# Kernel optimization log

Measured on AMD Instinct MI355X. Metric: run time of the kernel, lower is better.

Reference implementation:

```python
import jax, jax.numpy as jnp
import numpy as np

L = 6    # num_coupling_layers
D = 128  # input_dim
H = 16   # hidden width (output_dim in Coupling)
B = 131072


def setup_inputs() -> dict:
    key = jax.random.key(0)
    ks = jax.random.split(key, 32)
    half = D // 2
    m0 = np.concatenate([np.zeros(half), np.ones(half)])  # mask for even layers
    masks = jnp.asarray(np.stack([m0, 1.0 - m0] * (L // 2)), dtype=jnp.float32)  # [L, D]

    def glorot(k, shape):
        fan_in, fan_out = shape[-2], shape[-1]
        lim = np.sqrt(6.0 / (fan_in + fan_out)).astype(np.float32)
        return jax.random.uniform(k, shape, jnp.float32, -lim, lim)

    inp = {"x": jax.random.normal(ks[0], (B, D), jnp.float32), "masks": masks}
    ki = 1
    for p in ("t", "s"):
        for j, (din, dout) in enumerate([(D, H), (H, H), (H, H), (H, H), (H, D)], start=1):
            inp[f"{p}W{j}"] = glorot(ks[ki], (L, din, dout)); ki += 1
            inp[f"{p}b{j}"] = jnp.zeros((L, dout), jnp.float32)
    return inp


def _net(h, W1, b1, W2, b2, W3, b3, W4, b4, W5, b5):
    # 4 relu Dense(16) layers + linear Dense(D) head
    for W, b in ((W1, b1), (W2, b2), (W3, b3), (W4, b4)):
        h = jax.nn.relu(h @ W + b)
    return h @ W5 + b5


def _forward(x, masks, tW1, tb1, tW2, tb2, tW3, tb3, tW4, tb4, tW5, tb5,
             sW1, sb1, sW2, sb2, sW3, sb3, sW4, sb4, sW5, sb5):
    # training=True => direction = -1, gate = -1, layers iterated in reverse
    params = (masks, tW1, tb1, tW2, tb2, tW3, tb3, tW4, tb4, tW5, tb5,
              sW1, sb1, sW2, sb2, sW3, sb3, sW4, sb4, sW5, sb5)
    rev = jax.tree_util.tree_map(lambda a: a[::-1], params)  # reversed layer order

    def body(carry, p):
        x, ld = carry
        mask = p[0]
        rm = 1.0 - mask                      # reversed_mask
        xm = x * mask                        # x_masked
        t = rm * _net(xm, *p[1:11])          # translate (linear head)
        s = rm * jnp.tanh(_net(xm, *p[11:21]))  # log-scale (tanh head)
        # x = rm*(x*exp(-s) + (-1)*t*exp(-1*s)) + xm  ==  rm*(x - t)*exp(-s) + xm
        x = rm * (x - t) * jnp.exp(-s) + xm
        ld = ld - jnp.sum(s, axis=1)         # log_det_inv += gate * sum(s), gate = -1
        return (x, ld), None

    (y, logdet), _ = jax.lax.scan(body, (x, jnp.zeros(x.shape[0], x.dtype)), rev)
    return y, logdet


def reference(x, masks, tW1, tb1, tW2, tb2, tW3, tb3, tW4, tb4, tW5, tb5,
              sW1, sb1, sW2, sb2, sW3, sb3, sW4, sb4, sW5, sb5):
    return _forward(x, masks, tW1, tb1, tW2, tb2, tW3, tb3, tW4, tb4, tW5, tb5,
                    sW1, sb1, sW2, sb2, sW3, sb3, sW4, sb4, sW5, sb5)
```

## Files before the change

### kernel.cpp

```cpp
#include <hip/hip_runtime.h>
#include <math.h>

#define NL 6
#define DD 128

typedef __bf16 bf16x8 __attribute__((ext_vector_type(8)));
typedef float  f32x4  __attribute__((ext_vector_type(4)));

#define NET_STRIDE 9216
#define OFF_HID    2048
#define OFF_HEAD   5120

static __device__ __forceinline__ unsigned cvt_pk_bf16(float lo, float hi){
    unsigned r;
    asm("v_cvt_pk_bf16_f32 %0, %1, %2" : "=v"(r) : "v"(lo), "v"(hi));
    return r;
}
static __device__ __forceinline__ f32x4 mfma(bf16x8 a, bf16x8 b, f32x4 c){
    return __builtin_amdgcn_mfma_f32_16x16x32_bf16(a, b, c, 0, 0, 0);
}
static __device__ __forceinline__ bf16x8 frag4(unsigned w0, unsigned w1, unsigned w2, unsigned w3){
    int4 v; v.x=(int)w0; v.y=(int)w1; v.z=(int)w2; v.w=(int)w3;
    return __builtin_bit_cast(bf16x8, v);
}
static __device__ __forceinline__ bf16x8 dreg_to_B(f32x4 d){
    unsigned w0 = cvt_pk_bf16(fmaxf(d[0],0.f), fmaxf(d[1],0.f));
    unsigned w1 = cvt_pk_bf16(fmaxf(d[2],0.f), fmaxf(d[3],0.f));
    return frag4(w0, w1, 0u, 0u);
}
static __device__ __forceinline__ bf16x8 load_frag(const unsigned char* nb, int off, int lane){
    return *(const bf16x8*)(nb + off + lane * 16);
}

static __device__ __forceinline__ unsigned short f2bf_rne(float f){
    unsigned u = __float_as_uint(f);
    u += 0x7FFFu + ((u >> 16) & 1u);
    return (unsigned short)(u >> 16);
}

__global__ void pack_frags(
    const float* __restrict__ tW1, const float* __restrict__ tW2,
    const float* __restrict__ tW3, const float* __restrict__ tW4,
    const float* __restrict__ tW5,
    const float* __restrict__ sW1, const float* __restrict__ sW2,
    const float* __restrict__ sW3, const float* __restrict__ sW4,
    const float* __restrict__ sW5,
    unsigned char* __restrict__ pw)
{
    const int bx = blockIdx.x;
    const int l = bx >> 1, p = bx & 1;
    const int aOff = (l & 1) ? 0 : 64;
    const int pOff = 64 - aOff;
    const float* W1 = p ? sW1 : tW1;
    const float* W2 = p ? sW2 : tW2;
    const float* W3 = p ? sW3 : tW3;
    const float* W4 = p ? sW4 : tW4;
    const float* W5 = p ? sW5 : tW5;
    unsigned char* base = pw + (size_t)bx * NET_STRIDE;

    for (int t = threadIdx.x; t < 576; t += blockDim.x){
        const int lane = t & 63, m = lane & 15, q = lane >> 4;
        unsigned short v[8];
        unsigned char* dst;
        if (t < 128){
            int slice = t >> 6;
            #pragma unroll
            for (int e = 0; e < 8; ++e){
                int sg = (e < 4) ? (4*q + e) : (16 + 4*q + (e - 4));
                v[e] = f2bf_rne(W1[l*2048 + (aOff + 32*slice + sg)*16 + m]);
            }
            dst = base + slice*1024 + lane*16;
        } else if (t < 320){
            int hh = (t - 128) >> 6;
            const float* W = (hh == 0) ? W2 : (hh == 1) ? W3 : W4;
            #pragma unroll
            for (int e = 0; e < 8; ++e)
                v[e] = (e < 4) ? f2bf_rne(W[l*256 + (4*q + e)*16 + m]) : (unsigned short)0;
            dst = base + OFF_HID + hh*1024 + lane*16;
        } else {
            int c = (t - 320) >> 6;
            #pragma unroll
            for (int e = 0; e < 8; ++e)
                v[e] = (e < 4) ? f2bf_rne(W5[l*2048 + (4*q + e)*128 + pOff + 16*c + m])
                               : (unsigned short)0;
            dst = base + OFF_HEAD + c*1024 + lane*16;
        }
        int4 o;
        o.x = (int)((unsigned)v[0] | ((unsigned)v[1] << 16));
        o.y = (int)((unsigned)v[2] | ((unsigned)v[3] << 16));
        o.z = (int)((unsigned)v[4] | ((unsigned)v[5] << 16));
        o.w = (int)((unsigned)v[6] | ((unsigned)v[7] << 16));
        *(int4*)dst = o;
    }
}

__global__ __launch_bounds__(256, 6)
void realnvp_mfma16(const float* __restrict__ X, const unsigned char* __restrict__ PW,
    const float* __restrict__ tb1, const float* __restrict__ tb2,
    const float* __restrict__ tb3, const float* __restrict__ tb4,
    const float* __restrict__ tb5,
    const float* __restrict__ sb1, const float* __restrict__ sb2,
    const float* __restrict__ sb3, const float* __restrict__ sb4,
    const float* __restrict__ sb5,
    float* __restrict__ Y, float* __restrict__ LD, int B)
{
    __shared__ float4 xpl[4][256];
    const int tid  = threadIdx.x;
    const int lane = tid & 63;
    const int wid  = blockIdx.x * 4 + (tid >> 6);
    const int q = lane >> 4, n = lane & 15;
    const int row = wid * 16 + n;
    if (wid * 16 >= B) return;
    const int rowc = (row < B) ? row : (B - 1);

    const float* xrow = X + (size_t)rowc * DD;
    float4 xa[4];
    #pragma unroll
    for (int j = 0; j < 4; ++j){
        const int off = 16*j + 4*q;
        xa[j]       = *(const float4*)(xrow + off);
        xpl[j][tid] = *(const float4*)(xrow + 64 + off);
    }
    float sacc = 0.f;

    #pragma unroll 1
    for (int step = 0; step < NL; ++step){
        const int l = NL - 1 - step;
        const int pOff = (l & 1) ? 64 : 0;
        const unsigned char* bt = PW + (size_t)(l * 2 + 0) * NET_STRIDE;
        const unsigned char* bs = PW + (size_t)(l * 2 + 1) * NET_STRIDE;

        bf16x8 Bt0 = frag4(cvt_pk_bf16(xa[0].x, xa[0].y), cvt_pk_bf16(xa[0].z, xa[0].w),
                           cvt_pk_bf16(xa[1].x, xa[1].y), cvt_pk_bf16(xa[1].z, xa[1].w));
        bf16x8 Bt1 = frag4(cvt_pk_bf16(xa[2].x, xa[2].y), cvt_pk_bf16(xa[2].z, xa[2].w),
                           cvt_pk_bf16(xa[3].x, xa[3].y), cvt_pk_bf16(xa[3].z, xa[3].w));

        f32x4 at = *(const f32x4*)(tb1 + l*16 + 4*q);
        f32x4 as = *(const f32x4*)(sb1 + l*16 + 4*q);
        at = mfma(load_frag(bt, 0,    lane), Bt0, at);
        at = mfma(load_frag(bt, 1024, lane), Bt1, at);
        as = mfma(load_frag(bs, 0,    lane), Bt0, as);
        as = mfma(load_frag(bs, 1024, lane), Bt1, as);

        #pragma unroll
        for (int hh = 0; hh < 3; ++hh){
            const float* hbt = (hh == 0) ? tb2 : (hh == 1) ? tb3 : tb4;
            const float* hbs = (hh == 0) ? sb2 : (hh == 1) ? sb3 : sb4;
            bf16x8 Bh_t = dreg_to_B(at);
            bf16x8 Bh_s = dreg_to_B(as);
            at = mfma(load_frag(bt, OFF_HID + hh*1024, lane), Bh_t,
                      *(const f32x4*)(hbt + l*16 + 4*q));
            as = mfma(load_frag(bs, OFF_HID + hh*1024, lane), Bh_s,
                      *(const f32x4*)(hbs + l*16 + 4*q));
        }

        bf16x8 Bf_t = dreg_to_B(at);
        bf16x8 Bf_s = dreg_to_B(as);
        #pragma unroll
        for (int c = 0; c < 4; ++c){
            f32x4 ct = *(const f32x4*)(tb5 + l*128 + pOff + 16*c + 4*q);
            f32x4 cs = *(const f32x4*)(sb5 + l*128 + pOff + 16*c + 4*q);
            f32x4 tD = mfma(load_frag(bt, OFF_HEAD + c*1024, lane), Bf_t, ct);
            f32x4 sD = mfma(load_frag(bs, OFF_HEAD + c*1024, lane), Bf_s, cs);

            float4 xpv = xpl[c][tid];
            float xq[4] = {xpv.x, xpv.y, xpv.z, xpv.w};
            float nv[4];
            #pragma unroll
            for (int r = 0; r < 4; ++r){
                float u  = exp2f(sD[r] * 2.885390081777927f);
                float rr = __builtin_amdgcn_rcpf(u + 1.f);
                float se = fmaf(-2.f, rr, 1.f);
                float e  = exp2f(fmaf(rr, 2.885390081777927f,
                                      -1.4426950408889634f));
                nv[r] = (xq[r] - tD[r]) * e;
                sacc += se;
            }
            xpl[c][tid] = xa[c];
            xa[c] = (float4){nv[0], nv[1], nv[2], nv[3]};
        }
    }

    if (row < B){
        float* yrow = Y + (size_t)row * DD;
        #pragma unroll
        for (int j = 0; j < 4; ++j){
            const int off = 16*j + 4*q;
            *(float4*)(yrow + off)      = xa[j];
            *(float4*)(yrow + 64 + off) = xpl[j][tid];
        }
        float ls = sacc;
        ls += __shfl_xor(ls, 16, 64);
        ls += __shfl_xor(ls, 32, 64);
        if (q == 0) LD[row] = -ls;
    }
}

extern "C" void kernel_launch(void* const* d_in, const int* in_sizes, int n_in,
                              void* d_out, int out_size, void* d_ws, size_t ws_size,
                              hipStream_t stream)
{
    const float* X   = (const float*)d_in[0];
    const float* tW1 = (const float*)d_in[2];  const float* tb1 = (const float*)d_in[3];
    const float* tW2 = (const float*)d_in[4];  const float* tb2 = (const float*)d_in[5];
    const float* tW3 = (const float*)d_in[6];  const float* tb3 = (const float*)d_in[7];
    const float* tW4 = (const float*)d_in[8];  const float* tb4 = (const float*)d_in[9];
    const float* tW5 = (const float*)d_in[10]; const float* tb5 = (const float*)d_in[11];
    const float* sW1 = (const float*)d_in[12]; const float* sb1 = (const float*)d_in[13];
    const float* sW2 = (const float*)d_in[14]; const float* sb2 = (const float*)d_in[15];
    const float* sW3 = (const float*)d_in[16]; const float* sb3 = (const float*)d_in[17];
    const float* sW4 = (const float*)d_in[18]; const float* sb4 = (const float*)d_in[19];
    const float* sW5 = (const float*)d_in[20]; const float* sb5 = (const float*)d_in[21];

    const int B = in_sizes[0] / DD;
    float* Y  = (float*)d_out;
    float* LD = Y + (size_t)B * DD;

    unsigned char* pw = (unsigned char*)d_ws;
    hipLaunchKernelGGL(pack_frags, dim3(NL * 2), dim3(256), 0, stream,
                       tW1, tW2, tW3, tW4, tW5, sW1, sW2, sW3, sW4, sW5, pw);

    const int nwaves = (B + 15) / 16;
    const int blocks = (nwaves + 3) / 4;
    hipLaunchKernelGGL(realnvp_mfma16, dim3(blocks), dim3(256), 0, stream,
                       X, pw, tb1, tb2, tb3, tb4, tb5, sb1, sb2, sb3, sb4, sb5,
                       Y, LD, B);
}
```

Before: 77.37 us.

## Process two 16-row tiles per wave to reuse weight fragments

Each wave now handles 32 rows as two 16-row MFMA tiles. Every weight fragment loaded from the packed buffer feeds two MFMAs, and the two tiles give independent dependency chains that can hide MFMA latency. The cost is higher register and LDS use per wave: shared memory doubles and launch bounds drop from 6 to 4 blocks per CU, so occupancy falls and fewer waves are launched in total.

```diff
diff --git a/kernel.cpp b/kernel.cpp
--- a/kernel.cpp
+++ b/kernel.cpp
@@ -30,6 +30,23 @@
 }
 static __device__ __forceinline__ bf16x8 load_frag(const unsigned char* nb, int off, int lane){
     return *(const bf16x8*)(nb + off + lane * 16);
+}
+static __device__ __forceinline__ void epi(f32x4 tD, f32x4 sD,
+                                           float4 &xa, float4 &xp, float &sacc){
+    float xq[4] = {xp.x, xp.y, xp.z, xp.w};
+    float nv[4];
+    #pragma unroll
+    for (int r = 0; r < 4; ++r){
+        float u  = exp2f(sD[r] * 2.885390081777927f);
+        float rr = __builtin_amdgcn_rcpf(u + 1.f);
+        float se = fmaf(-2.f, rr, 1.f);
+        float e  = exp2f(fmaf(rr, 2.885390081777927f,
+                              -1.4426950408889634f));
+        nv[r] = (xq[r] - tD[r]) * e;
+        sacc += se;
+    }
+    xp = xa;
+    xa = (float4){nv[0], nv[1], nv[2], nv[3]};
 }
 
 static __device__ __forceinline__ unsigned short f2bf_rne(float f){
@@ -94,8 +111,8 @@
     }
 }
 
-__global__ __launch_bounds__(256, 6)
-void realnvp_mfma16(const float* __restrict__ X, const unsigned char* __restrict__ PW,
+__global__ __launch_bounds__(256, 4)
+void realnvp_mfma16x2(const float* __restrict__ X, const unsigned char* __restrict__ PW,
     const float* __restrict__ tb1, const float* __restrict__ tb2,
     const float* __restrict__ tb3, const float* __restrict__ tb4,
     const float* __restrict__ tb5,
@@ -104,24 +121,29 @@
     const float* __restrict__ sb5,
     float* __restrict__ Y, float* __restrict__ LD, int B)
 {
-    __shared__ float4 xpl[4][256];
+    __shared__ float4 xpl[8][256];
     const int tid  = threadIdx.x;
     const int lane = tid & 63;
     const int wid  = blockIdx.x * 4 + (tid >> 6);
     const int q = lane >> 4, n = lane & 15;
-    const int row = wid * 16 + n;
-    if (wid * 16 >= B) return;
-    const int rowc = (row < B) ? row : (B - 1);
-
-    const float* xrow = X + (size_t)rowc * DD;
-    float4 xa[4];
+    const int r0 = wid * 32 + n;
+    const int r1 = r0 + 16;
+    if (wid * 32 >= B) return;
+    const int r0c = (r0 < B) ? r0 : (B - 1);
+    const int r1c = (r1 < B) ? r1 : (B - 1);
+
+    const float* x0 = X + (size_t)r0c * DD;
+    const float* x1 = X + (size_t)r1c * DD;
+    float4 xa0[4], xa1[4];
     #pragma unroll
     for (int j = 0; j < 4; ++j){
         const int off = 16*j + 4*q;
-        xa[j]       = *(const float4*)(xrow + off);
-        xpl[j][tid] = *(const float4*)(xrow + 64 + off);
-    }
-    float sacc = 0.f;
+        xa0[j]          = *(const float4*)(x0 + off);
+        xpl[j][tid]     = *(const float4*)(x0 + 64 + off);
+        xa1[j]          = *(const float4*)(x1 + off);
+        xpl[4 + j][tid] = *(const float4*)(x1 + 64 + off);
+    }
+    float sacc0 = 0.f, sacc1 = 0.f;
 
     #pragma unroll 1
     for (int step = 0; step < NL; ++step){
@@ -130,69 +152,86 @@
         const unsigned char* bt = PW + (size_t)(l * 2 + 0) * NET_STRIDE;
         const unsigned char* bs = PW + (size_t)(l * 2 + 1) * NET_STRIDE;
 
-        bf16x8 Bt0 = frag4(cvt_pk_bf16(xa[0].x, xa[0].y), cvt_pk_bf16(xa[0].z, xa[0].w),
-                           cvt_pk_bf16(xa[1].x, xa[1].y), cvt_pk_bf16(xa[1].z, xa[1].w));
-        bf16x8 Bt1 = frag4(cvt_pk_bf16(xa[2].x, xa[2].y), cvt_pk_bf16(xa[2].z, xa[2].w),
-                           cvt_pk_bf16(xa[3].x, xa[3].y), cvt_pk_bf16(xa[3].z, xa[3].w));
-
-        f32x4 at = *(const f32x4*)(tb1 + l*16 + 4*q);
-        f32x4 as = *(const f32x4*)(sb1 + l*16 + 4*q);
-        at = mfma(load_frag(bt, 0,    lane), Bt0, at);
-        at = mfma(load_frag(bt, 1024, lane), Bt1, at);
-        as = mfma(load_frag(bs, 0,    lane), Bt0, as);
-        as = mfma(load_frag(bs, 1024, lane), Bt1, as);
+        bf16x8 B00 = frag4(cvt_pk_bf16(xa0[0].x, xa0[0].y), cvt_pk_bf16(xa0[0].z, xa0[0].w),
+                           cvt_pk_bf16(xa0[1].x, xa0[1].y), cvt_pk_bf16(xa0[1].z, xa0[1].w));
+        bf16x8 B01 = frag4(cvt_pk_bf16(xa0[2].x, xa0[2].y), cvt_pk_bf16(xa0[2].z, xa0[2].w),
+                           cvt_pk_bf16(xa0[3].x, xa0[3].y), cvt_pk_bf16(xa0[3].z, xa0[3].w));
+        bf16x8 B10 = frag4(cvt_pk_bf16(xa1[0].x, xa1[0].y), cvt_pk_bf16(xa1[0].z, xa1[0].w),
+                           cvt_pk_bf16(xa1[1].x, xa1[1].y), cvt_pk_bf16(xa1[1].z, xa1[1].w));
+        bf16x8 B11 = frag4(cvt_pk_bf16(xa1[2].x, xa1[2].y), cvt_pk_bf16(xa1[2].z, xa1[2].w),
+                           cvt_pk_bf16(xa1[3].x, xa1[3].y), cvt_pk_bf16(xa1[3].z, xa1[3].w));
+
+        f32x4 cbt = *(const f32x4*)(tb1 + l*16 + 4*q);
+        f32x4 cbs = *(const f32x4*)(sb1 + l*16 + 4*q);
+        bf16x8 A0t = load_frag(bt, 0, lane), A1t = load_frag(bt, 1024, lane);
+        bf16x8 A0s = load_frag(bs, 0, lane), A1s = load_frag(bs, 1024, lane);
+        f32x4 at0 = mfma(A0t, B00, cbt); at0 = mfma(A1t, B01, at0);
+        f32x4 at1 = mfma(A0t, B10, cbt); at1 = mfma(A1t, B11, at1);
+        f32x4 as0 = mfma(A0s, B00, cbs); as0 = mfma(A1s, B01, as0);
+        f32x4 as1 = mfma(A0s, B10, cbs); as1 = mfma(A1s, B11, as1);
 
         #pragma unroll
         for (int hh = 0; hh < 3; ++hh){
             const float* hbt = (hh == 0) ? tb2 : (hh == 1) ? tb3 : tb4;
             const float* hbs = (hh == 0) ? sb2 : (hh == 1) ? sb3 : sb4;
-            bf16x8 Bh_t = dreg_to_B(at);
-            bf16x8 Bh_s = dreg_to_B(as);
-            at = mfma(load_frag(bt, OFF_HID + hh*1024, lane), Bh_t,
-                      *(const f32x4*)(hbt + l*16 + 4*q));
-            as = mfma(load_frag(bs, OFF_HID + hh*1024, lane), Bh_s,
-                      *(const f32x4*)(hbs + l*16 + 4*q));
-        }
-
-        bf16x8 Bf_t = dreg_to_B(at);
-        bf16x8 Bf_s = dreg_to_B(as);
+            f32x4 ct = *(const f32x4*)(hbt + l*16 + 4*q);
+            f32x4 cs = *(const f32x4*)(hbs + l*16 + 4*q);
+            bf16x8 At = load_frag(bt, OFF_HID + hh*1024, lane);
+            bf16x8 As = load_frag(bs, OFF_HID + hh*1024, lane);
+            at0 = mfma(At, dreg_to_B(at0), ct);
+            at1 = mfma(At, dreg_to_B(at1), ct);
+            as0 = mfma(As, dreg_to_B(as0), cs);
+            as1 = mfma(As, dreg_to_B(as1), cs);
+        }
+
+        bf16x8 Bf_t0 = dreg_to_B(at0), Bf_t1 = dreg_to_B(at1);
+        bf16x8 Bf_s0 = dreg_to_B(as0), Bf_s1 = dreg_to_B(as1);
         #pragma unroll
         for (int c = 0; c < 4; ++c){
             f32x4 ct = *(const f32x4*)(tb5 + l*128 + pOff + 16*c + 4*q);
             f32x4 cs = *(const f32x4*)(sb5 + l*128 + pOff + 16*c + 4*q);
-            f32x4 tD = mfma(load_frag(bt, OFF_HEAD + c*1024, lane), Bf_t, ct);
-            f32x4 sD = mfma(load_frag(bs, OFF_HEAD + c*1024, lane), Bf_s, cs);
-
-            float4 xpv = xpl[c][tid];
-            float xq[4] = {xpv.x, xpv.y, xpv.z, xpv.w};
-            float nv[4];
-            #pragma unroll
-            for (int r = 0; r < 4; ++r){
-                float u  = exp2f(sD[r] * 2.885390081777927f);
-                float rr = __builtin_amdgcn_rcpf(u + 1.f);
-                float se = fmaf(-2.f, rr, 1.f);
-                float e  = exp2f(fmaf(rr, 2.885390081777927f,
-                                      -1.4426950408889634f));
-                nv[r] = (xq[r] - tD[r]) * e;
-                sacc += se;
-            }
-            xpl[c][tid] = xa[c];
-            xa[c] = (float4){nv[0], nv[1], nv[2], nv[3]};
-        }
-    }
-
-    if (row < B){
-        float* yrow = Y + (size_t)row * DD;
+            bf16x8 Aht = load_frag(bt, OFF_HEAD + c*1024, lane);
+            bf16x8 Ahs = load_frag(bs, OFF_HEAD + c*1024, lane);
+            f32x4 tD0 = mfma(Aht, Bf_t0, ct);
+            f32x4 sD0 = mfma(Ahs, Bf_s0, cs);
+            f32x4 tD1 = mfma(Aht, Bf_t1, ct);
+            f32x4 sD1 = mfma(Ahs, Bf_s1, cs);
+
+            float4 xp0 = xpl[c][tid];
+            epi(tD0, sD0, xa0[c], xp0, sacc0);
+            xpl[c][tid] = xp0;
+
+            float4 xp1 = xpl[4 + c][tid];
+            epi(tD1, sD1, xa1[c], xp1, sacc1);
+            xpl[4 + c][tid] = xp1;
+        }
+    }
+
+    if (r0 < B){
+        float* y0 = Y + (size_t)r0 * DD;
         #pragma unroll
         for (int j = 0; j < 4; ++j){
             const int off = 16*j + 4*q;
-            *(float4*)(yrow + off)      = xa[j];
-            *(float4*)(yrow + 64 + off) = xpl[j][tid];
-        }
-        float ls = sacc;
+            *(float4*)(y0 + off)      = xa0[j];
+            *(float4*)(y0 + 64 + off) = xpl[j][tid];
+        }
+        float ls = sacc0;
         ls += __shfl_xor(ls, 16, 64);
         ls += __shfl_xor(ls, 32, 64);
-        if (q == 0) LD[row] = -ls;
+        if (q == 0) LD[r0] = -ls;
+    }
+    if (r1 < B){
+        float* y1 = Y + (size_t)r1 * DD;
+        #pragma unroll
+        for (int j = 0; j < 4; ++j){
+            const int off = 16*j + 4*q;
+            *(float4*)(y1 + off)      = xa1[j];
+            *(float4*)(y1 + 64 + off) = xpl[4 + j][tid];
+        }
+        float ls = sacc1;
+        ls += __shfl_xor(ls, 16, 64);
+        ls += __shfl_xor(ls, 32, 64);
+        if (q == 0) LD[r1] = -ls;
     }
 }
 
@@ -220,9 +259,9 @@
     hipLaunchKernelGGL(pack_frags, dim3(NL * 2), dim3(256), 0, stream,
                        tW1, tW2, tW3, tW4, tW5, sW1, sW2, sW3, sW4, sW5, pw);
 
-    const int nwaves = (B + 15) / 16;
+    const int nwaves = (B + 31) / 32;
     const int blocks = (nwaves + 3) / 4;
-    hipLaunchKernelGGL(realnvp_mfma16, dim3(blocks), dim3(256), 0, stream,
+    hipLaunchKernelGGL(realnvp_mfma16x2, dim3(blocks), dim3(256), 0, stream,
                        X, pw, tb1, tb2, tb3, tb4, tb5, sb1, sb2, sb3, sb4, sb5,
                        Y, LD, B);
 }
```

Result: faster. 72.27 us (-6.6%).
